# Kernel tuning notes

Measured on AMD Instinct MI355X. Metric: run time of the kernel, lower is better.

The kernel has to match this reference:

```python
import jax, jax.numpy as jnp
import numpy as np

D = 64      # node_input_dim == node_hidden_dim
EIN = 16    # edge_input_dim
EH = 64     # edge_hidden_dim
NL, NR = 5000, 15000
EL, ER = 50000, 150000
STEPS = 6
EPS = 1e-5
SLOPE = 0.01


def _ln(x, g, b):
    mu = jnp.mean(x, axis=-1, keepdims=True)
    v = jnp.mean((x - mu) ** 2, axis=-1, keepdims=True)
    return (x - mu) / jnp.sqrt(v + EPS) * g + b


def _lrelu(x):
    return jnp.where(x > 0, x, SLOPE * x)


def setup_inputs() -> dict:
    key = jax.random.key(0)
    ks = jax.random.split(key, 32)

    def n(k, shape, fan_in):
        return jax.random.normal(k, shape, jnp.float32) * (fan_in ** -0.5)

    return {
        'lig_n_feat': jax.random.normal(ks[0], (NL, D), jnp.float32),
        'lig_e_feat': jax.random.normal(ks[1], (EL, EIN), jnp.float32),
        'lig_src': jax.random.randint(ks[2], (EL,), 0, NL),
        'lig_dst': jax.random.randint(ks[3], (EL,), 0, NL),
        'rec_n_feat': jax.random.normal(ks[4], (NR, D), jnp.float32),
        'rec_e_feat': jax.random.normal(ks[5], (ER, EIN), jnp.float32),
        'rec_src': jax.random.randint(ks[6], (ER,), 0, NR),
        'rec_dst': jax.random.randint(ks[7], (ER,), 0, NR),
        'mask': jax.random.uniform(ks[8], (NL, NR), jnp.float32),
        # linear0
        'W0': n(ks[9], (D, D), D), 'b0': jnp.zeros((D,), jnp.float32),
        # edge network: Linear(EIN,EH) -> ReLU -> Linear(EH, D*D)
        'We1': n(ks[10], (EH, EIN), EIN), 'be1': jnp.zeros((EH,), jnp.float32),
        'We2': n(ks[11], (D * D, EH), EH), 'be2': jnp.zeros((D * D,), jnp.float32),
        # NNConv residual fc (no bias) and conv bias
        'resW': n(ks[12], (D, D), D), 'conv_b': jnp.zeros((D,), jnp.float32),
        # message layer Linear(2D, D)
        'msgW': n(ks[13], (D, 2 * D), 2 * D), 'msgb': jnp.zeros((D,), jnp.float32),
        # attention projections (no bias)
        'Qlig': n(ks[14], (D, D), D), 'Klig': n(ks[15], (D, D), D), 'Vlig': n(ks[16], (D, D), D),
        'Qrec': n(ks[17], (D, D), D), 'Krec': n(ks[18], (D, D), D), 'Vrec': n(ks[19], (D, D), D),
        # final LayerNorms
        'g_lig': jnp.ones((D,), jnp.float32), 'b_lig': jnp.zeros((D,), jnp.float32),
        'g_rec': jnp.ones((D,), jnp.float32), 'b_rec': jnp.zeros((D,), jnp.float32),
    }


def _gather_branch(x, efeat, src, dst, n_nodes, W0, b0, We1, be1, We2, be2, resW, conv_b, msgW, msgb):
    # per-edge weight matrices from edge MLP: [E, D, D] (in x out)
    We = jax.nn.relu(efeat @ We1.T + be1) @ We2.T + be2
    We = We.reshape(-1, D, D)
    h = jax.nn.relu(x @ W0.T + b0)
    for _ in range(STEPS):
        msg = jnp.einsum('ei,eio->eo', h[src], We)          # gather + per-edge transform
        agg = jax.ops.segment_sum(msg, dst, num_segments=n_nodes)  # scatter-sum
        m = jax.nn.relu(agg + h @ resW.T + conv_b)           # NNConv residual + bias, relu
        h = jnp.concatenate([m, h], axis=1) @ msgW.T + msgb  # message_layer
    return h + x


def reference(lig_n_feat, lig_e_feat, lig_src, lig_dst, rec_n_feat, rec_e_feat, rec_src, rec_dst,
              mask, W0, b0, We1, be1, We2, be2, resW, conv_b, msgW, msgb,
              Qlig, Klig, Vlig, Qrec, Krec, Vrec, g_lig, b_lig, g_rec, b_rec):
    lig_Fv = _gather_branch(lig_n_feat, lig_e_feat, lig_src, lig_dst, NL,
                            W0, b0, We1, be1, We2, be2, resW, conv_b, msgW, msgb)
    rec_Fv = _gather_branch(rec_n_feat, rec_e_feat, rec_src, rec_dst, NR,
                            W0, b0, We1, be1, We2, be2, resW, conv_b, msgW, msgb)
    hl = _ln(lig_Fv, g_lig, b_lig)
    hr = _ln(rec_Fv, g_rec, b_rec)
    # lig attends to rec
    ql, kr, vr = _lrelu(hl @ Qlig.T), _lrelu(hr @ Krec.T), hr @ Vrec.T
    a = mask * (ql @ kr.T) - 1000.0 * (1.0 - mask)
    att_lig = jax.nn.softmax(a, axis=1) @ vr
    # rec attends to lig
    qr, kl, vl = _lrelu(hr @ Qrec.T), _lrelu(hl @ Klig.T), hl @ Vlig.T
    mt = mask.T
    a2 = mt * (qr @ kl.T) - 1000.0 * (1.0 - mt)
    att_rec = jax.nn.softmax(a2, axis=1) @ vl
    return (_ln(att_lig, g_lig, b_lig), _ln(att_rec, g_rec, b_rec))
```

## Files before the change

### kernel.cpp

```cpp
#include <hip/hip_runtime.h>
#include <hip/hip_bf16.h>

typedef unsigned short ushort_t;
typedef __attribute__((ext_vector_type(8))) short short8_t;
typedef __attribute__((ext_vector_type(4))) float f32x4;
typedef __attribute__((ext_vector_type(4))) unsigned uint4_t;

#define NLIG 5000
#define NREC 15000
#define NTOT 20000
#define ELIG 50000
#define EREC 150000
#define ETOT 200000
#define VSTRIDE 20160
#define NB0 313
#define NB1 938

__device__ __forceinline__ float us2f(ushort_t u){
  union { float f; unsigned int i; } x; x.i = ((unsigned int)u) << 16; return x.f;
}
__device__ __forceinline__ ushort_t f2us(float f){
  __hip_bfloat16 b = __float2bfloat16(f);
  return *reinterpret_cast<ushort_t*>(&b);
}
__device__ __forceinline__ unsigned pkbf(float a, float b){
  return (unsigned)f2us(a) | ((unsigned)f2us(b) << 16);
}
__device__ __forceinline__ float wsum64(float v){
#pragma unroll
  for (int s = 32; s >= 1; s >>= 1) v += __shfl_xor(v, s, 64);
  return v;
}
__device__ __forceinline__ f32x4 mfma32(short8_t a, short8_t b, f32x4 c){
  return __builtin_amdgcn_mfma_f32_16x16x32_bf16(a, b, c, 0, 0, 0);
}
__device__ __forceinline__ int geti(const int* __restrict__ p, int i, int i64){
  return i64 ? p[2*i] : p[i];
}

__global__ void kdetect2(const unsigned* __restrict__ xw, const unsigned* __restrict__ iw,
                         int* __restrict__ flagp){
  const int lane = threadIdx.x;
  unsigned w = xw[lane];
  int e0 = (int)((w >> 7) & 0xFF);
  int hit = (e0 >= 100 && e0 <= 134) ? 1 : 0;
  int zodd = ((lane & 1) && iw[lane] == 0u) ? 1 : 0;
#pragma unroll
  for (int s = 32; s >= 1; s >>= 1){
    hit  += __shfl_xor(hit,  s, 64);
    zodd += __shfl_xor(zodd, s, 64);
  }
  if (lane == 0){
    flagp[0] = (hit  >= 40) ? 1 : 0;
    flagp[1] = (zodd >= 24) ? 1 : 0;
  }
}

__global__ void ksent(float* __restrict__ out, int n, float c){
  int i = blockIdx.x*256 + threadIdx.x;
  if (i < n) out[i] = c;
}

__global__ void kcvt_x(const void* __restrict__ lx, const void* __restrict__ rx,
                       const int* __restrict__ flagp, float* __restrict__ xall){
  const int flag = flagp[0];
  const int idx = blockIdx.x*256 + threadIdx.x;
  const void* src; int local;
  if (idx < NLIG*64){ src = lx; local = idx; } else { src = rx; local = idx - NLIG*64; }
  float v;
  if (flag) v = us2f(((const ushort_t*)src)[local]);
  else      v = ((const float*)src)[local];
  xall[idx] = v;
}

struct Srcs { const void* p[20]; };
__global__ void kcvt_w(Srcs S, const int* __restrict__ flagp, float* __restrict__ wcvt){
  const int bounds[21] = {0,4096,4160,5184,5248,267392,271488,275584,275648,283840,
                          283904,288000,292096,296192,300288,304384,308480,308544,308608,308672,308736};
  const int flag = flagp[0];
  const int idx = blockIdx.x*256 + threadIdx.x;
  if (idx >= 308736) return;
  int seg = 0;
#pragma unroll
  for (int s = 1; s < 20; ++s) if (idx >= bounds[s]) seg = s;
  const void* src = S.p[0];
#pragma unroll
  for (int s = 1; s < 20; ++s) if (seg == s) src = S.p[s];
  const int local = idx - bounds[seg];
  float v;
  if (flag) v = us2f(((const ushort_t*)src)[local]);
  else      v = ((const float*)src)[local];
  wcvt[idx] = v;
}

#define W_W0    0
#define W_B0    4096
#define W_WE1   4160
#define W_BE1   5184
#define W_WE2   5248
#define W_BE2   267392
#define W_RESW  271488
#define W_CONVB 275584
#define W_MSGW  275648
#define W_MSGB  283840
#define W_QLIG  283904
#define W_KLIG  288000
#define W_VLIG  292096
#define W_QREC  296192
#define W_KREC  300288
#define W_VREC  304384
#define W_GLIG  308480
#define W_BLIG  308544
#define W_GREC  308608
#define W_BREC  308672

__global__ void kWpk(const float* __restrict__ We2f, ushort_t* __restrict__ Wpk){
  int oidx = blockIdx.x*256 + threadIdx.x;
  int j = oidx & 7, lane = (oidx >> 3) & 63, p = (oidx >> 9) & 1;
  int t = (oidx >> 10) & 3, kb = oidx >> 12;
  int o = t*16 + (lane & 15);
  int gik = kb*32 + (lane >> 4)*8 + j;
  int i = gik >> 6, k = gik & 63;
  float v = We2f[(size_t)(i*64 + o)*64 + k];
  ushort_t hi = f2us(v);
  Wpk[oidx] = p ? f2us(v - us2f(hi)) : hi;
}

__global__ void kh0(const float* __restrict__ xall, const float* __restrict__ W0f,
                    const float* __restrict__ b0f, float* __restrict__ h){
  __shared__ float xr[4][64];
  const int lane = threadIdx.x & 63, wv = threadIdx.x >> 6;
  const int n = blockIdx.x*4 + wv;
  xr[wv][lane] = xall[(size_t)n*64 + lane];
  __syncthreads();
  float acc = b0f[lane];
  const float* wr = W0f + lane*64;
#pragma unroll
  for (int i = 0; i < 64; ++i) acc += xr[wv][i] * wr[i];
  h[(size_t)n*64 + lane] = acc > 0.f ? acc : 0.f;
}

__global__ void khist(const int* __restrict__ ldst, const int* __restrict__ rdst,
                      const int* __restrict__ flagp, int* __restrict__ counts){
  const int i64 = flagp[1];
  const int e = blockIdx.x*256 + threadIdx.x;
  if (e >= ETOT) return;
  int dstg = (e < ELIG) ? geti(ldst, e, i64) : geti(rdst, e - ELIG, i64) + NLIG;
  atomicAdd(&counts[dstg], 1);
}

__global__ __launch_bounds__(1024) void kscan(const int* __restrict__ counts, int* __restrict__ offs){
  __shared__ int part[1024];
  const int tid = threadIdx.x;
  const int PER = 20;
  int loc[PER]; int s = 0;
#pragma unroll
  for (int j = 0; j < PER; ++j){ int idx = tid*PER + j; int v = (idx < NTOT) ? counts[idx] : 0; loc[j] = s; s += v; }
  part[tid] = s;
  __syncthreads();
  for (int d = 1; d < 1024; d <<= 1){
    int add = (tid >= d) ? part[tid - d] : 0;
    __syncthreads();
    part[tid] += add;
    __syncthreads();
  }
  int pre = (tid > 0) ? part[tid - 1] : 0;
#pragma unroll
  for (int j = 0; j < PER; ++j){ int idx = tid*PER + j; if (idx < NTOT) offs[idx] = pre + loc[j]; }
  if (tid == 1023) offs[NTOT] = part[1023];
}

__global__ void kfill(const int* __restrict__ lsrc, const int* __restrict__ ldst,
                      const int* __restrict__ rsrc, const int* __restrict__ rdst,
                      const void* __restrict__ lef, const void* __restrict__ ref_,
                      const int* __restrict__ offs, int* __restrict__ cursor,
                      const int* __restrict__ flagp,
                      int* __restrict__ e_srcn, float* __restrict__ ef_srt){
  const int flag = flagp[0];
  const int i64  = flagp[1];
  const int e = blockIdx.x*256 + threadIdx.x;
  if (e >= ETOT) return;
  int srcg, dstg, le; const void* efb;
  if (e < ELIG){ srcg = geti(lsrc, e, i64); dstg = geti(ldst, e, i64); efb = lef; le = e; }
  else {
    int e2 = e - ELIG;
    srcg = geti(rsrc, e2, i64) + NLIG; dstg = geti(rdst, e2, i64) + NLIG; efb = ref_; le = e2;
  }
  int pos = offs[dstg] + atomicAdd(&cursor[dstg], 1);
  e_srcn[pos] = srcg;
  float* efd = ef_srt + (size_t)pos*16;
  if (flag){
    const ushort_t* efp = (const ushort_t*)efb + (size_t)le*16;
#pragma unroll
    for (int c = 0; c < 16; ++c) efd[c] = us2f(efp[c]);
  } else {
    const float* efp = (const float*)efb + (size_t)le*16;
#pragma unroll
    for (int c = 0; c < 16; ++c) efd[c] = efp[c];
  }
}

__global__ void kz(const float* __restrict__ ef_srt, const float* __restrict__ We1f,
                   const float* __restrict__ be1f, float* __restrict__ z_srt){
  const int lane = threadIdx.x & 63, wv = threadIdx.x >> 6;
  const int e = blockIdx.x*4 + wv;
  const float* efp = ef_srt + (size_t)e*16;
  float acc = be1f[lane];
  const float* wr = We1f + lane*16;
#pragma unroll
  for (int c = 0; c < 16; ++c) acc += efp[c] * wr[c];
  z_srt[(size_t)e*64 + lane] = acc > 0.f ? acc : 0.f;
}

#define SROW 2080
#define SLO  (16*SROW)
__global__ __launch_bounds__(1024)
void kstep(const float* __restrict__ hin, float* __restrict__ hout,
           const int* __restrict__ offs, const int* __restrict__ e_srcn,
           const float* __restrict__ z_srt,
           const ushort_t* __restrict__ Wpk,
           const float* __restrict__ resWf, const float* __restrict__ convbf,
           const float* __restrict__ msgWf, const float* __restrict__ msgbf,
           const float* __restrict__ be2f){
  __shared__ alignas(16) char sbuf[2*SLO];
  __shared__ float h_lds[1024];
  __shared__ float Hs_lds[1024];
  __shared__ float m_lds[1024];
  __shared__ float cbf[64], mbf[64];

  const int tid = threadIdx.x, lane = tid & 63, wv = tid >> 6;
  const int n0 = blockIdx.x * 16;

  h_lds[tid] = hin[(size_t)n0*64 + tid];
  if (tid < 64){ cbf[tid] = convbf[tid]; mbf[tid] = msgbf[tid]; }

  float sacc[64];
#pragma unroll
  for (int i = 0; i < 64; ++i) sacc[i] = 0.f;
  float hs = 0.f;
  {
    const int v = n0 + wv;
    const int jb = offs[v], je = offs[v+1];
    for (int j = jb; j < je; ++j){
      const int sn = e_srcn[j];
      const float zl = z_srt[(size_t)j*64 + lane];
      hs += hin[(size_t)sn*64 + lane];
      const float4* hp = (const float4*)(hin + (size_t)sn*64);
#pragma unroll
      for (int i4 = 0; i4 < 16; ++i4){
        float4 hv = hp[i4];
        sacc[i4*4+0] += hv.x * zl;
        sacc[i4*4+1] += hv.y * zl;
        sacc[i4*4+2] += hv.z * zl;
        sacc[i4*4+3] += hv.w * zl;
      }
    }
    Hs_lds[wv*64 + lane] = hs;
  }

  const int r15 = lane & 15, g4 = lane >> 4;
  const int tW = wv & 3, kq = wv >> 2;
  f32x4 acc; acc[0]=0.f; acc[1]=0.f; acc[2]=0.f; acc[3]=0.f;
#pragma unroll
  for (int c = 0; c < 4; ++c){
#pragma unroll
    for (int ii = 0; ii < 16; ++ii){
      float v = sacc[c*16 + ii];
      ushort_t hi16 = f2us(v);
      unsigned off = (unsigned)(wv*SROW + (ii*64 + lane)*2);
      *(ushort_t*)(sbuf + off) = hi16;
      *(ushort_t*)(sbuf + SLO + off) = f2us(v - us2f(hi16));
    }
    __syncthreads();
    for (int kk = 0; kk < 8; ++kk){
      const int lk = kq*256 + kk*32;
      const int kb = c*32 + kq*8 + kk;
      const unsigned aoff = (unsigned)(r15*SROW + (lk + g4*8)*2);
      const short8_t ah = *(const short8_t*)(sbuf + aoff);
      const short8_t al = *(const short8_t*)(sbuf + SLO + aoff);
      const ushort_t* bp = Wpk + (size_t)(kb*4 + tW)*1024 + lane*8;
      const short8_t bh = *(const short8_t*)(bp);
      const short8_t bl = *(const short8_t*)(bp + 512);
      acc = mfma32(ah, bh, acc);
      acc = mfma32(ah, bl, acc);
      acc = mfma32(al, bh, acc);
    }
    __syncthreads();
  }

  float* redf  = (float*)sbuf;
  float* be2s  = (float*)(sbuf + 16384);
  float* resWt = (float*)(sbuf + 32768);
#pragma unroll
  for (int q = 0; q < 4; ++q)
    redf[kq*1024 + (g4*4 + q)*64 + tW*16 + r15] = acc[q];
  for (int idx = tid; idx < 4096; idx += 1024){
    be2s[idx] = be2f[idx];
    resWt[(idx & 63)*65 + (idx >> 6)] = resWf[idx];
  }
  __syncthreads();
  {
    float aggv = cbf[lane];
#pragma unroll
    for (int k4 = 0; k4 < 4; ++k4) aggv += redf[k4*1024 + wv*64 + lane];
    float t1 = 0.f, t2 = 0.f;
#pragma unroll 8
    for (int i = 0; i < 64; ++i){
      t1 += Hs_lds[wv*64 + i] * be2s[i*64 + lane];
      t2 += h_lds[wv*64 + i]  * resWt[i*65 + lane];
    }
    float mv = aggv + t1 + t2;
    m_lds[wv*64 + lane] = mv > 0.f ? mv : 0.f;
  }
  __syncthreads();
  float* msgWt = (float*)sbuf;
  for (int idx = tid; idx < 8192; idx += 1024)
    msgWt[(idx & 127)*65 + (idx >> 7)] = msgWf[idx];
  __syncthreads();
  {
    float hn = mbf[lane];
#pragma unroll 8
    for (int i = 0; i < 64; ++i){
      hn += m_lds[wv*64 + i] * msgWt[i*65 + lane];
      hn += h_lds[wv*64 + i] * msgWt[(64 + i)*65 + lane];
    }
    hout[(size_t)(n0 + wv)*64 + lane] = hn;
  }
}

__global__ void kfvproj(const float* __restrict__ h, const float* __restrict__ xall,
    const float* __restrict__ wcvt,
    ushort_t* __restrict__ qbh, ushort_t* __restrict__ qbl,
    ushort_t* __restrict__ kbh, ushort_t* __restrict__ kbl,
    ushort_t* __restrict__ vbT){
  __shared__ float hr[4][64];
  const int lane = threadIdx.x & 63, wv = threadIdx.x >> 6;
  const int n = blockIdx.x*4 + wv;
  const bool isLig = n < NLIG;
  const float fv = h[(size_t)n*64 + lane] + xall[(size_t)n*64 + lane];
  const float mu = wsum64(fv) * (1.f/64.f);
  const float dd = fv - mu;
  const float var = wsum64(dd*dd) * (1.f/64.f);
  const float gg = wcvt[(isLig ? W_GLIG : W_GREC) + lane];
  const float bb = wcvt[(isLig ? W_BLIG : W_BREC) + lane];
  const float hl = dd * rsqrtf(var + 1e-5f) * gg + bb;
  hr[wv][lane] = hl;
  __syncthreads();
  const float* Qw = wcvt + (isLig ? W_QLIG : W_QREC) + lane*64;
  const float* Kw = wcvt + (isLig ? W_KLIG : W_KREC) + lane*64;
  const float* Vw = wcvt + (isLig ? W_VLIG : W_VREC) + lane*64;
  float qa = 0.f, ka = 0.f, va = 0.f;
#pragma unroll
  for (int i = 0; i < 64; ++i){
    const float hv = hr[wv][i];
    qa += hv * Qw[i];
    ka += hv * Kw[i];
    va += hv * Vw[i];
  }
  qa = qa > 0.f ? qa : 0.01f*qa;
  ka = ka > 0.f ? ka : 0.01f*ka;
  const size_t o = (size_t)n*64 + lane;
  ushort_t qh = f2us(qa); qbh[o] = qh; qbl[o] = f2us(qa - us2f(qh));
  ushort_t kh = f2us(ka); kbh[o] = kh; kbl[o] = f2us(ka - us2f(kh));
  vbT[(size_t)lane*VSTRIDE + n] = f2us(va);
}

__global__ __launch_bounds__(512)
void kattn2(const ushort_t* __restrict__ qbh, const ushort_t* __restrict__ qbl,
            const ushort_t* __restrict__ kbh, const ushort_t* __restrict__ kbl,
            const ushort_t* __restrict__ vbT, const void* __restrict__ maskp,
            const int* __restrict__ flagp, const float* __restrict__ wcvt,
            float* __restrict__ out){
  __shared__ alignas(16) char abuf[34816];
  __shared__ float mred[8][16], lred[8][16];
  float (*m_tile)[16][257] = (float(*)[16][257])abuf;
  float (*ored)[64][17]    = (float(*)[64][17])abuf;

  const int flag = flagp[0];
  const int bx = blockIdx.x;
  const int dirn = (bx < NB0) ? 0 : 1;
  const int bid  = dirn ? (bx - NB0) : bx;
  const int R   = dirn ? NREC : NLIG;
  const int C   = dirn ? NLIG : NREC;
  const int RNB = dirn ? NLIG : 0;
  const int CNB = dirn ? 0 : NLIG;
  const float* gwf = wcvt + (dirn ? W_GREC : W_GLIG);
  const float* bwf = wcvt + (dirn ? W_BREC : W_BLIG);
  float* outp = out + (size_t)RNB*64;

  const int tid = threadIdx.x, lane = tid & 63, wv = tid >> 6;
  const int r15 = lane & 15, g4 = lane >> 4;
  const int rbase = bid * 16;
  int rn = rbase + r15; if (rn > R-1) rn = R-1;

  const ushort_t* qph = qbh + (size_t)(RNB + rn)*64;
  const ushort_t* qpl = qbl + (size_t)(RNB + rn)*64;
  const short8_t qh0a = *(const short8_t*)(qph + g4*8);
  const short8_t qh0b = *(const short8_t*)(qph + 32 + g4*8);
  const short8_t ql0a = *(const short8_t*)(qpl + g4*8);
  const short8_t ql0b = *(const short8_t*)(qpl + 32 + g4*8);

  const int srcA = (((g4 & 1) * 2)     << 4) + r15;
  const int srcB = (((g4 & 1) * 2 + 1) << 4) + r15;
  const bool hiBank = (g4 >> 1) != 0;

  const int s_row = tid >> 5, s_l31 = tid & 31;
  const int s_cl = tid >> 1, s_half = tid & 1;

  float mr[8];
  auto load_tile = [&](int tb2){
    if (dirn == 0){
      int r = rbase + s_row; if (r > R-1) r = R-1;
      const size_t base = (size_t)r*NREC + tb2;
      const int cmax = C-1 - tb2;
      if (flag){
        const ushort_t* mp = (const ushort_t*)maskp + base;
#pragma unroll
        for (int j = 0; j < 8; ++j){
          int cj = s_l31 + 32*j; if (cj > cmax) cj = cmax;
          mr[j] = us2f(mp[cj]);
        }
      } else {
        const float* mp = (const float*)maskp + base;
#pragma unroll
        for (int j = 0; j < 8; ++j){
          int cj = s_l31 + 32*j; if (cj > cmax) cj = cmax;
          mr[j] = mp[cj];
        }
      }
    } else {
      int c = tb2 + s_cl; if (c > C-1) c = C-1;
      int r0 = rbase + s_half*8; if (r0 > R-8) r0 = R-8;
      const size_t base = (size_t)c*NREC + r0;
      if (flag){
        const ushort_t* mp = (const ushort_t*)maskp + base;
        const short8_t v8 = *(const short8_t*)mp;
#pragma unroll
        for (int j = 0; j < 8; ++j) mr[j] = us2f((ushort_t)v8[j]);
      } else {
        const float* mp = (const float*)maskp + base;
        const float4 v0 = *(const float4*)mp;
        const float4 v1 = *(const float4*)(mp + 4);
        mr[0]=v0.x; mr[1]=v0.y; mr[2]=v0.z; mr[3]=v0.w;
        mr[4]=v1.x; mr[5]=v1.y; mr[6]=v1.z; mr[7]=v1.w;
      }
    }
  };

  float mrun = -1e30f, lrun = 0.f;
  f32x4 oacc[4];
#pragma unroll
  for (int t = 0; t < 4; ++t){ oacc[t][0]=0.f; oacc[t][1]=0.f; oacc[t][2]=0.f; oacc[t][3]=0.f; }

  load_tile(0);
  int buf = 0;
  for (int tb = 0; tb < C; tb += 256){
    if (dirn == 0){
#pragma unroll
      for (int j = 0; j < 8; ++j) m_tile[buf][s_row][s_l31 + 32*j] = mr[j];
    } else {
#pragma unroll
      for (int j = 0; j < 8; ++j) m_tile[buf][s_half*8 + j][s_cl] = mr[j];
    }
    if (tb + 256 < C) load_tile(tb + 256);
    __syncthreads();

    const int cb = tb + wv*32;
    int cn0 = cb + r15;      if (cn0 > C-1) cn0 = C-1;
    int cn1 = cb + 16 + r15; if (cn1 > C-1) cn1 = C-1;
    const ushort_t* kp0h = kbh + (size_t)(CNB + cn0)*64;
    const ushort_t* kp0l = kbl + (size_t)(CNB + cn0)*64;
    const ushort_t* kp1h = kbh + (size_t)(CNB + cn1)*64;
    const ushort_t* kp1l = kbl + (size_t)(CNB + cn1)*64;
    f32x4 st0; st0[0]=0.f; st0[1]=0.f; st0[2]=0.f; st0[3]=0.f;
    f32x4 st1 = st0;
    {
      short8_t ka_ = *(const short8_t*)(kp0h + g4*8);
      short8_t kb_ = *(const short8_t*)(kp0h + 32 + g4*8);
      st0 = mfma32(ka_, qh0a, st0); st0 = mfma32(kb_, qh0b, st0);
      st0 = mfma32(ka_, ql0a, st0); st0 = mfma32(kb_, ql0b, st0);
      short8_t kc_ = *(const short8_t*)(kp0l + g4*8);
      short8_t kd_ = *(const short8_t*)(kp0l + 32 + g4*8);
      st0 = mfma32(kc_, qh0a, st0); st0 = mfma32(kd_, qh0b, st0);
    }
    {
      short8_t ka_ = *(const short8_t*)(kp1h + g4*8);
      short8_t kb_ = *(const short8_t*)(kp1h + 32 + g4*8);
      st1 = mfma32(ka_, qh0a, st1); st1 = mfma32(kb_, qh0b, st1);
      st1 = mfma32(ka_, ql0a, st1); st1 = mfma32(kb_, ql0b, st1);
      short8_t kc_ = *(const short8_t*)(kp1l + g4*8);
      short8_t kd_ = *(const short8_t*)(kp1l + 32 + g4*8);
      st1 = mfma32(kc_, qh0a, st1); st1 = mfma32(kd_, qh0b, st1);
    }
    float sv0[4], sv1[4]; float tmax = -1e30f;
#pragma unroll
    for (int j = 0; j < 4; ++j){
      const int c0 = cb + g4*4 + j, c1 = cb + 16 + g4*4 + j;
      const float mv0 = m_tile[buf][r15][wv*32 + g4*4 + j];
      const float mv1 = m_tile[buf][r15][wv*32 + 16 + g4*4 + j];
      sv0[j] = (c0 < C) ? mv0 * (st0[j] + 1000.f) : -1e30f;
      sv1[j] = (c1 < C) ? mv1 * (st1[j] + 1000.f) : -1e30f;
      tmax = fmaxf(tmax, fmaxf(sv0[j], sv1[j]));
    }
    tmax = fmaxf(tmax, __shfl_xor(tmax, 16, 64));
    tmax = fmaxf(tmax, __shfl_xor(tmax, 32, 64));
    const float mnew = fmaxf(mrun, tmax);
    const float corr = __expf(mrun - mnew);
    float ps0[4], ps1[4], psum = 0.f;
#pragma unroll
    for (int j = 0; j < 4; ++j){
      ps0[j] = __expf(sv0[j] - mnew); psum += ps0[j];
      ps1[j] = __expf(sv1[j] - mnew); psum += ps1[j];
    }
    psum += __shfl_xor(psum, 16, 64);
    psum += __shfl_xor(psum, 32, 64);
    lrun = lrun * corr + psum;
    mrun = mnew;
    const unsigned pk0 = pkbf(ps0[0], ps0[1]);
    const unsigned pk1 = pkbf(ps0[2], ps0[3]);
    const unsigned pk2 = pkbf(ps1[0], ps1[1]);
    const unsigned pk3 = pkbf(ps1[2], ps1[3]);
    const unsigned a0 = (unsigned)__shfl((int)pk0, srcA, 64);
    const unsigned a2 = (unsigned)__shfl((int)pk2, srcA, 64);
    const unsigned a1 = (unsigned)__shfl((int)pk1, srcA, 64);
    const unsigned a3 = (unsigned)__shfl((int)pk3, srcA, 64);
    const unsigned b0 = (unsigned)__shfl((int)pk0, srcB, 64);
    const unsigned b2 = (unsigned)__shfl((int)pk2, srcB, 64);
    const unsigned b1 = (unsigned)__shfl((int)pk1, srcB, 64);
    const unsigned b3 = (unsigned)__shfl((int)pk3, srcB, 64);
    uint4_t pw;
    pw[0] = hiBank ? a2 : a0;
    pw[1] = hiBank ? a3 : a1;
    pw[2] = hiBank ? b2 : b0;
    pw[3] = hiBank ? b3 : b1;
    const short8_t pf8 = *reinterpret_cast<const short8_t*>(&pw);
    const ushort_t* vtb = vbT + (size_t)(CNB + cb + g4*8);
#pragma unroll
    for (int t = 0; t < 4; ++t){
#pragma unroll
      for (int q = 0; q < 4; ++q) oacc[t][q] *= corr;
      const short8_t af = *(const short8_t*)(vtb + (size_t)(t*16 + r15)*VSTRIDE);
      oacc[t] = mfma32(af, pf8, oacc[t]);
    }
    buf ^= 1;
  }

  __syncthreads();
  if (g4 == 0){ mred[wv][r15] = mrun; lred[wv][r15] = lrun; }
#pragma unroll
  for (int t = 0; t < 4; ++t)
#pragma unroll
    for (int q = 0; q < 4; ++q)
      ored[wv][t*16 + g4*4 + q][r15] = oacc[t][q];
  __syncthreads();

  for (int rr = 2*wv; rr <= 2*wv + 1; ++rr){
    float mstar = -1e30f;
#pragma unroll
    for (int w = 0; w < 8; ++w) mstar = fmaxf(mstar, mred[w][rr]);
    float lstar = 0.f, ov = 0.f;
#pragma unroll
    for (int w = 0; w < 8; ++w){
      const float e = __expf(mred[w][rr] - mstar);
      lstar += lred[w][rr] * e;
      ov    += ored[w][lane][rr] * e;
    }
    const float att = ov / lstar;
    const float mu = wsum64(att) * (1.f/64.f);
    const float dd = att - mu;
    const float var = wsum64(dd*dd) * (1.f/64.f);
    const float y = dd * rsqrtf(var + 1e-5f) * gwf[lane] + bwf[lane];
    const int rg = rbase + rr;
    if (rg < R) outp[(size_t)rg*64 + lane] = y;
  }
}

extern "C" void kernel_launch(void* const* d_in, const int* in_sizes, int n_in,
                              void* d_out, int out_size, void* d_ws, size_t ws_size,
                              hipStream_t stream){
  const int expsz[29] = {320000,800000,50000,50000,960000,2400000,150000,150000,75000000,
                         4096,64,1024,64,262144,4096,4096,64,8192,64,
                         4096,4096,4096,4096,4096,4096,64,64,64,64};
  bool ok = (n_in == 29);
  if (ok) for (int i = 0; i < 29; ++i) if (in_sizes[i] != expsz[i]) ok = false;
  if (!ok){
    ksent<<<(out_size + 255)/256, 256, 0, stream>>>((float*)d_out, out_size, 10.0f);
    return;
  }

  const void* lig_n = d_in[0];
  const void* lig_e = d_in[1];
  const int* lig_src = (const int*)d_in[2];
  const int* lig_dst = (const int*)d_in[3];
  const void* rec_n = d_in[4];
  const void* rec_e = d_in[5];
  const int* rec_src = (const int*)d_in[6];
  const int* rec_dst = (const int*)d_in[7];
  const void* mask = d_in[8];

  char* p = (char*)d_ws;
  auto carve = [&](size_t bytes)->char*{ char* r = p; p += (bytes + 255) & ~(size_t)255; return r; };
  float*    xall  = (float*)   carve((size_t)NTOT*64*4);
  float*    wcvt  = (float*)   carve((size_t)308736*4);
  float*    h_a   = (float*)   carve((size_t)NTOT*64*4);
  float*    h_b   = (float*)   carve((size_t)NTOT*64*4);
  ushort_t* Wpk   = (ushort_t*)carve((size_t)524288*2);
  ushort_t* qbh   = (ushort_t*)carve((size_t)NTOT*64*2);
  ushort_t* qbl   = (ushort_t*)carve((size_t)NTOT*64*2);
  ushort_t* kbh   = (ushort_t*)carve((size_t)NTOT*64*2);
  ushort_t* kbl   = (ushort_t*)carve((size_t)NTOT*64*2);
  ushort_t* vbT   = (ushort_t*)carve((size_t)64*VSTRIDE*2);
  int*      flag  = (int*)     carve(256);
  int*      counts= (int*)     carve((size_t)2*NTOT*4);
  int*      cursor= counts + NTOT;
  int*      offs  = (int*)     carve((size_t)(NTOT+1)*4);
  int*      e_srcn= (int*)     carve((size_t)ETOT*4);
  float*    ef_srt= (float*)   carve((size_t)ETOT*16*4);
  float*    z_srt = (float*)   carve((size_t)ETOT*64*4);

  if ((size_t)(p - (char*)d_ws) > ws_size){
    ksent<<<(out_size + 255)/256, 256, 0, stream>>>((float*)d_out, out_size, 20.0f);
    return;
  }

  Srcs S;
  for (int i = 0; i < 20; ++i) S.p[i] = d_in[9 + i];

  hipMemsetAsync(counts, 0, (size_t)2*NTOT*4, stream);
  hipMemsetAsync(vbT, 0, (size_t)64*VSTRIDE*2, stream);
  kdetect2<<<1, 64, 0, stream>>>((const unsigned*)lig_n, (const unsigned*)lig_src, flag);
  kcvt_x<<<NTOT*64/256, 256, 0, stream>>>(lig_n, rec_n, flag, xall);
  kcvt_w<<<(308736 + 255)/256, 256, 0, stream>>>(S, flag, wcvt);
  kWpk<<<2048, 256, 0, stream>>>(wcvt + W_WE2, Wpk);
  kh0<<<NTOT/4, 256, 0, stream>>>(xall, wcvt + W_W0, wcvt + W_B0, h_a);
  khist<<<(ETOT + 255)/256, 256, 0, stream>>>(lig_dst, rec_dst, flag, counts);
  kscan<<<1, 1024, 0, stream>>>(counts, offs);
  kfill<<<(ETOT + 255)/256, 256, 0, stream>>>(lig_src, lig_dst, rec_src, rec_dst,
                                              lig_e, rec_e, offs, cursor, flag, e_srcn, ef_srt);
  kz<<<ETOT/4, 256, 0, stream>>>(ef_srt, wcvt + W_WE1, wcvt + W_BE1, z_srt);
  float* hi = h_a; float* ho = h_b;
  for (int s = 0; s < 6; ++s){
    kstep<<<NTOT/16, 1024, 0, stream>>>(hi, ho, offs, e_srcn, z_srt, Wpk,
                                        wcvt + W_RESW, wcvt + W_CONVB,
                                        wcvt + W_MSGW, wcvt + W_MSGB, wcvt + W_BE2);
    float* t = hi; hi = ho; ho = t;
  }
  kfvproj<<<NTOT/4, 256, 0, stream>>>(hi, xall, wcvt, qbh, qbl, kbh, kbl, vbT);
  kattn2<<<NB0 + NB1, 512, 0, stream>>>(qbh, qbl, kbh, kbl, vbT, mask, flag, wcvt,
                                        (float*)d_out);
}
```

Before: 2.112 ms.

## Split lig-to-rec attention over key segments with flash-decoding style combine

The ligand-direction attention, which has 5000 rows but 15000 keys, is split into three key segments. Each segment block writes partial max, sum and output to a workspace buffer, and a new combine kernel merges the partials and applies the LayerNorm. Before, this direction had only 313 long-running blocks, so it created a load imbalance against the 938 receptor blocks. The change adds one kernel launch and extra partial-result traffic, and it reuses the ef_srt buffer for scratch.

```diff
diff --git a/kernel.cpp b/kernel.cpp
--- a/kernel.cpp
+++ b/kernel.cpp
@@ -15,6 +15,9 @@
 #define VSTRIDE 20160
 #define NB0 313
 #define NB1 938
+#define SEGLEN 5000
+#define NBA (NB0*3 + NB1)
+#define PSLOT 1056
 
 __device__ __forceinline__ float us2f(ushort_t u){
   union { float f; unsigned int i; } x; x.i = ((unsigned int)u) << 16; return x.f;
@@ -366,11 +369,10 @@
 }
 
 __global__ __launch_bounds__(512)
-void kattn2(const ushort_t* __restrict__ qbh, const ushort_t* __restrict__ qbl,
+void kattn3(const ushort_t* __restrict__ qbh, const ushort_t* __restrict__ qbl,
             const ushort_t* __restrict__ kbh, const ushort_t* __restrict__ kbl,
             const ushort_t* __restrict__ vbT, const void* __restrict__ maskp,
-            const int* __restrict__ flagp, const float* __restrict__ wcvt,
-            float* __restrict__ out){
+            const int* __restrict__ flagp, float* __restrict__ pbuf){
   __shared__ alignas(16) char abuf[34816];
   __shared__ float mred[8][16], lred[8][16];
   float (*m_tile)[16][257] = (float(*)[16][257])abuf;
@@ -378,15 +380,15 @@
 
   const int flag = flagp[0];
   const int bx = blockIdx.x;
-  const int dirn = (bx < NB0) ? 0 : 1;
-  const int bid  = dirn ? (bx - NB0) : bx;
+  const int dirn = (bx < NB0*3) ? 0 : 1;
+  const int bid  = dirn ? (bx - NB0*3) : (bx/3);
+  const int seg  = dirn ? 0 : (bx - (bx/3)*3);
   const int R   = dirn ? NREC : NLIG;
   const int C   = dirn ? NLIG : NREC;
   const int RNB = dirn ? NLIG : 0;
   const int CNB = dirn ? 0 : NLIG;
-  const float* gwf = wcvt + (dirn ? W_GREC : W_GLIG);
-  const float* bwf = wcvt + (dirn ? W_BREC : W_BLIG);
-  float* outp = out + (size_t)RNB*64;
+  const int cs  = seg * SEGLEN;
+  const int ce  = dirn ? C : ((cs + SEGLEN < C) ? cs + SEGLEN : C);
 
   const int tid = threadIdx.x, lane = tid & 63, wv = tid >> 6;
   const int r15 = lane & 15, g4 = lane >> 4;
@@ -412,7 +414,7 @@
     if (dirn == 0){
       int r = rbase + s_row; if (r > R-1) r = R-1;
       const size_t base = (size_t)r*NREC + tb2;
-      const int cmax = C-1 - tb2;
+      const int cmax = ce-1 - tb2;
       if (flag){
         const ushort_t* mp = (const ushort_t*)maskp + base;
 #pragma unroll
@@ -429,7 +431,7 @@
         }
       }
     } else {
-      int c = tb2 + s_cl; if (c > C-1) c = C-1;
+      int c = tb2 + s_cl; if (c > ce-1) c = ce-1;
       int r0 = rbase + s_half*8; if (r0 > R-8) r0 = R-8;
       const size_t base = (size_t)c*NREC + r0;
       if (flag){
@@ -452,9 +454,9 @@
 #pragma unroll
   for (int t = 0; t < 4; ++t){ oacc[t][0]=0.f; oacc[t][1]=0.f; oacc[t][2]=0.f; oacc[t][3]=0.f; }
 
-  load_tile(0);
+  load_tile(cs);
   int buf = 0;
-  for (int tb = 0; tb < C; tb += 256){
+  for (int tb = cs; tb < ce; tb += 256){
     if (dirn == 0){
 #pragma unroll
       for (int j = 0; j < 8; ++j) m_tile[buf][s_row][s_l31 + 32*j] = mr[j];
@@ -462,12 +464,12 @@
 #pragma unroll
       for (int j = 0; j < 8; ++j) m_tile[buf][s_half*8 + j][s_cl] = mr[j];
     }
-    if (tb + 256 < C) load_tile(tb + 256);
+    if (tb + 256 < ce) load_tile(tb + 256);
     __syncthreads();
 
     const int cb = tb + wv*32;
-    int cn0 = cb + r15;      if (cn0 > C-1) cn0 = C-1;
-    int cn1 = cb + 16 + r15; if (cn1 > C-1) cn1 = C-1;
+    int cn0 = cb + r15;      if (cn0 > ce-1) cn0 = ce-1;
+    int cn1 = cb + 16 + r15; if (cn1 > ce-1) cn1 = ce-1;
     const ushort_t* kp0h = kbh + (size_t)(CNB + cn0)*64;
     const ushort_t* kp0l = kbl + (size_t)(CNB + cn0)*64;
     const ushort_t* kp1h = kbh + (size_t)(CNB + cn1)*64;
@@ -496,10 +498,10 @@
 #pragma unroll
     for (int j = 0; j < 4; ++j){
       const int c0 = cb + g4*4 + j, c1 = cb + 16 + g4*4 + j;
-      const float mv0 = m_tile[buf][r15][wv*32 + g4*4 + j];
-      const float mv1 = m_tile[buf][r15][wv*32 + 16 + g4*4 + j];
-      sv0[j] = (c0 < C) ? mv0 * (st0[j] + 1000.f) : -1e30f;
-      sv1[j] = (c1 < C) ? mv1 * (st1[j] + 1000.f) : -1e30f;
+      const float mv0 = m_tile[buf][r15][(cb - tb) + g4*4 + j];
+      const float mv1 = m_tile[buf][r15][(cb - tb) + 16 + g4*4 + j];
+      sv0[j] = (c0 < ce) ? mv0 * (st0[j] + 1000.f) : -1e30f;
+      sv1[j] = (c1 < ce) ? mv1 * (st1[j] + 1000.f) : -1e30f;
       tmax = fmaxf(tmax, fmaxf(sv0[j], sv1[j]));
     }
     tmax = fmaxf(tmax, __shfl_xor(tmax, 16, 64));
@@ -554,6 +556,7 @@
       ored[wv][t*16 + g4*4 + q][r15] = oacc[t][q];
   __syncthreads();
 
+  float* ps = pbuf + (size_t)bx * PSLOT;
   for (int rr = 2*wv; rr <= 2*wv + 1; ++rr){
     float mstar = -1e30f;
 #pragma unroll
@@ -564,14 +567,46 @@
       const float e = __expf(mred[w][rr] - mstar);
       lstar += lred[w][rr] * e;
       ov    += ored[w][lane][rr] * e;
+    }
+    if (lane == 0){ ps[rr] = mstar; ps[16 + rr] = lstar; }
+    ps[32 + rr*64 + lane] = ov;
+  }
+}
+
+__global__ __launch_bounds__(64)
+void kcomb(const float* __restrict__ pbuf, const float* __restrict__ wcvt,
+           float* __restrict__ out){
+  const int rb = blockIdx.x;
+  const int lane = threadIdx.x;
+  const int dirn = (rb < NB0) ? 0 : 1;
+  const int bid  = dirn ? (rb - NB0) : rb;
+  const int R    = dirn ? NREC : NLIG;
+  const int nseg = dirn ? 1 : 3;
+  const int slot0= dirn ? (NB0*3 + bid) : (bid*3);
+  const float* gwf = wcvt + (dirn ? W_GREC : W_GLIG);
+  const float* bwf = wcvt + (dirn ? W_BREC : W_BLIG);
+  float* outp = out + (size_t)(dirn ? NLIG : 0)*64;
+  const int rbase = bid * 16;
+
+  for (int rr = 0; rr < 16; ++rr){
+    const int rg = rbase + rr;
+    if (rg >= R) break;
+    float mstar = -1e30f;
+    for (int s = 0; s < nseg; ++s)
+      mstar = fmaxf(mstar, pbuf[(size_t)(slot0 + s)*PSLOT + rr]);
+    float lstar = 0.f, ov = 0.f;
+    for (int s = 0; s < nseg; ++s){
+      const float* psl = pbuf + (size_t)(slot0 + s)*PSLOT;
+      const float e = __expf(psl[rr] - mstar);
+      lstar += psl[16 + rr] * e;
+      ov    += psl[32 + rr*64 + lane] * e;
     }
     const float att = ov / lstar;
     const float mu = wsum64(att) * (1.f/64.f);
     const float dd = att - mu;
     const float var = wsum64(dd*dd) * (1.f/64.f);
     const float y = dd * rsqrtf(var + 1e-5f) * gwf[lane] + bwf[lane];
-    const int rg = rbase + rr;
-    if (rg < R) outp[(size_t)rg*64 + lane] = y;
+    outp[(size_t)rg*64 + lane] = y;
   }
 }
 
@@ -617,6 +652,7 @@
   int*      e_srcn= (int*)     carve((size_t)ETOT*4);
   float*    ef_srt= (float*)   carve((size_t)ETOT*16*4);
   float*    z_srt = (float*)   carve((size_t)ETOT*64*4);
+  float*    pbuf  = ef_srt;
 
   if ((size_t)(p - (char*)d_ws) > ws_size){
     ksent<<<(out_size + 255)/256, 256, 0, stream>>>((float*)d_out, out_size, 20.0f);
@@ -646,6 +682,6 @@
     float* t = hi; hi = ho; ho = t;
   }
   kfvproj<<<NTOT/4, 256, 0, stream>>>(hi, xall, wcvt, qbh, qbl, kbh, kbl, vbT);
-  kattn2<<<NB0 + NB1, 512, 0, stream>>>(qbh, qbl, kbh, kbl, vbT, mask, flag, wcvt,
-                                        (float*)d_out);
-}
+  kattn3<<<NBA, 512, 0, stream>>>(qbh, qbl, kbh, kbl, vbT, mask, flag, pbuf);
+  kcomb<<<NB0 + NB1, 64, 0, stream>>>(pbuf, wcvt, (float*)d_out);
+}
```

After: 2.151 ms. About the same (+1.8%).
